# Kernel optimization log

Hardware: AMD Instinct MI355X
Metric: run time of the kernel (lower is better)

The kernel has to match this reference:

```python
import jax, jax.numpy as jnp
import numpy as np

N_NODES = 200000
N_EDGES = 6400000
HIDDEN = 200
N_HID_LAYERS = 6  # 8-layer MLP: in + 6 hidden + out


def setup_inputs() -> dict:
    key = jax.random.key(0)
    ks = jax.random.split(key, 12)
    x = jax.random.normal(ks[0], (N_NODES, 1), dtype=jnp.float32)
    edge_index = jax.random.randint(ks[1], (2, N_EDGES), 0, N_NODES, dtype=jnp.int64)
    # GraphConv(1,1): lin_rel (with bias) applied to aggregated neighbors, lin_root (no bias)
    w_rel = jax.random.normal(ks[2], (1, 1), dtype=jnp.float32)
    b_rel = jax.random.normal(ks[3], (1,), dtype=jnp.float32) * 0.1
    w_root = jax.random.normal(ks[4], (1, 1), dtype=jnp.float32)
    # MLP(1, 200, 1, num_layers=8)
    w_in = jax.random.normal(ks[5], (1, HIDDEN), dtype=jnp.float32) * (1.0 / 1.0)
    b_in = jnp.zeros((HIDDEN,), dtype=jnp.float32)
    w_hid = jax.random.normal(ks[6], (N_HID_LAYERS, HIDDEN, HIDDEN), dtype=jnp.float32) * (1.0 / np.sqrt(HIDDEN))
    b_hid = jnp.zeros((N_HID_LAYERS, HIDDEN), dtype=jnp.float32)
    w_out = jax.random.normal(ks[7], (HIDDEN, 1), dtype=jnp.float32) * (1.0 / np.sqrt(HIDDEN))
    b_out = jnp.zeros((1,), dtype=jnp.float32)
    return {
        "x": x, "edge_index": edge_index,
        "w_rel": w_rel, "b_rel": b_rel, "w_root": w_root,
        "w_in": w_in, "b_in": b_in,
        "w_hid": w_hid, "b_hid": b_hid,
        "w_out": w_out, "b_out": b_out,
    }


def reference(x, edge_index, w_rel, b_rel, w_root, w_in, b_in, w_hid, b_hid, w_out, b_out):
    # GraphConv with sum aggregation: out_i = W_rel @ sum_{j in N(i)} x_j + b_rel + W_root @ x_i
    src = edge_index[0]
    dst = edge_index[1]
    agg = jax.ops.segment_sum(x[src], dst, num_segments=N_NODES)  # [N, 1]
    h = agg @ w_rel + b_rel + x @ w_root                          # [N, 1]
    # 8-layer MLP with ReLU between layers
    h = jax.nn.relu(h @ w_in + b_in)                              # [N, 200]
    for i in range(N_HID_LAYERS):
        h = jax.nn.relu(h @ w_hid[i] + b_hid[i])
    h = h @ w_out + b_out                                         # [N, 1]
    return jax.nn.sigmoid(h)
```

## Files before the change

kernel.cpp:

```cpp
#include <hip/hip_runtime.h>

#define N_NODES 200000
#define N_EDGES 6400000
#define HID 200
#define NREP 8
#define MT 64
#define ASTR 232
#define AELEM (MT * ASTR)
#define WSTR 232
#define WROWS 224
#define WELEMS (WROWS * WSTR)
#define H0ROWS 112
#define H1ROWS 96
#define H0CH (H0ROWS * WSTR * 2 / 16)
#define H1CH (H1ROWS * WSTR * 2 / 16)

#define LDS_WOFF 29696
#define LDS_TOTAL 81664

#define NPART 20
#define PNODES 10000
#define PBLK 50
#define CHUNK_E (N_EDGES / PBLK)
#define APPLY_LDS (PNODES * 4)

typedef float f32x4 __attribute__((ext_vector_type(4)));
typedef _Float16 f16x8 __attribute__((ext_vector_type(8)));
typedef unsigned short u16;
typedef unsigned int u32;

__device__ __align__(16) float g_agg[N_NODES];
__device__ __align__(16) float g_xf8[NREP * N_NODES];
__device__ __align__(16) float g_wf[6 * HID * HID];
__device__ __align__(16) _Float16 g_wph[6 * WELEMS];
__device__ __align__(16) float g_ev[N_EDGES];
__device__ __align__(16) float g_part[NPART * PBLK * PNODES];
__device__ int g_isbf;

__device__ __forceinline__ float bf2f(u16 u) {
  union { u32 i; float f; } v; v.i = ((u32)u) << 16; return v.f;
}
__device__ __forceinline__ u16 f2bf(float f) {
  u32 i = __float_as_uint(f);
  return (u16)((i + 0x7FFFu + ((i >> 16) & 1u)) >> 16);
}
__device__ __forceinline__ float ldf(const void* p, int i, int isbf) {
  return isbf ? bf2f(((const u16*)p)[i]) : ((const float*)p)[i];
}
__device__ __forceinline__ void load_lds16(const void* g, void* l) {
  __builtin_amdgcn_global_load_lds(
      (const __attribute__((address_space(1))) u32*)g,
      (__attribute__((address_space(3))) u32*)l, 16, 0, 0);
}

constexpr int tf1(int m) { return (m & 3) + 1; }
constexpr int tf2(int m) { return ((m >> 2) & 3) + 2; }
constexpr int tg1(int k) { return (k & 7) + 1; }
constexpr int tg2(int k) { return ((k >> 3) & 3) + 1; }
constexpr int tu1(int k) { return ((k * 3) & 7) + 1; }
constexpr int tu2(int k) { return ((k >> 2) & 3) + 2; }
constexpr int tw1(int n) { return ((n * 5) & 7) + 1; }
constexpr int tw2(int n) { return ((n >> 2) & 3) + 1; }
constexpr int calcS(int i, int j) {
  int s = 0;
  for (int k = 0; k < 32; ++k)
    s += (i ? tg2(k) : tg1(k)) * (j ? tu2(k) : tu1(k));
  return s;
}
__device__ __forceinline__ float refD(int m, int n) {
  constexpr int S11 = calcS(0, 0), S12 = calcS(0, 1), S21 = calcS(1, 0), S22 = calcS(1, 1);
  return (float)(tf1(m) * tw1(n) * S11 + tf1(m) * tw2(n) * S12 +
                 tf2(m) * tw1(n) * S21 + tf2(m) * tw2(n) * S22);
}
__device__ int mfma_selftest(int l15, int q) {
  f16x8 av, bv;
#pragma unroll
  for (int j = 0; j < 8; ++j) {
    int k = q * 8 + j;
    av[j] = (_Float16)(float)(tf1(l15) * tg1(k) + tf2(l15) * tg2(k));
    bv[j] = (_Float16)(float)(tu1(k) * tw1(l15) + tu2(k) * tw2(l15));
  }
  f32x4 d = __builtin_amdgcn_mfma_f32_16x16x32_f16(av, bv, (f32x4){0.f, 0.f, 0.f, 0.f}, 0, 0, 0);
  bool ok0 = true, ok1 = true;
#pragma unroll
  for (int r = 0; r < 4; ++r) {
    ok0 = ok0 && (d[r] == refD(q * 4 + r, l15));
    ok1 = ok1 && (d[r] == refD(l15, q * 4 + r));
  }
  return __all(ok0) ? 0 : (__all(ok1) ? 1 : 2);
}

__global__ void sniff_kernel(const u32* __restrict__ xw) {
  int i = threadIdx.x;
  u32 e = (xw[i] >> 7) & 0xFFu;
  unsigned long long b = __ballot(e >= 110u && e <= 135u);
  if (i == 0) g_isbf = (__popcll(b) >= 48) ? 1 : 0;
}

__global__ void prep_kernel(const void* __restrict__ x, const void* __restrict__ w_hid) {
  int t = blockIdx.x * blockDim.x + threadIdx.x;
  int isbf = g_isbf;
  if (t < NREP * N_NODES) {
    int qd = t / N_NODES;
    int node = t - qd * N_NODES;
    g_xf8[t] = ldf(x, node, isbf);
  }
  if (t < 6 * HID * HID) g_wf[t] = ldf(w_hid, t, isbf);
  if (t < 6 * WELEMS) {
    int l = t / WELEMS;
    int r = t - l * WELEMS;
    int n = r / WSTR;
    int k = r - n * WSTR;
    float v = 0.f;
    if (n < HID && k < HID) v = ldf(w_hid, (l * HID + k) * HID + n, isbf);
    g_wph[t] = (_Float16)v;
  }
}

__global__ void gather_kernel(const int* __restrict__ ei) {
  int t = blockIdx.x * blockDim.x + threadIdx.x;
  int e = t * 8;
  int xcc;
  asm volatile("s_getreg_b32 %0, hwreg(HW_REG_XCC_ID)" : "=s"(xcc));
  const float* xf = g_xf8 + (size_t)(xcc & (NREP - 1)) * N_NODES;
  bool is64 = ((ei[1] | ei[3] | ei[5] | ei[7]) == 0);
  int s[8];
  if (is64) {
#pragma unroll
    for (int i = 0; i < 4; ++i) {
      int4 a = *(const int4*)(ei + 2 * e + 4 * i);
      s[2 * i] = a.x; s[2 * i + 1] = a.z;
    }
  } else {
#pragma unroll
    for (int i = 0; i < 2; ++i) {
      int4 a = *(const int4*)(ei + e + 4 * i);
      s[4 * i] = a.x; s[4 * i + 1] = a.y; s[4 * i + 2] = a.z; s[4 * i + 3] = a.w;
    }
  }
  float v[8];
#pragma unroll
  for (int i = 0; i < 8; ++i) v[i] = xf[s[i]];
  *(float4*)(g_ev + e) = (float4){v[0], v[1], v[2], v[3]};
  *(float4*)(g_ev + e + 4) = (float4){v[4], v[5], v[6], v[7]};
}

__global__ __launch_bounds__(256) void apply_kernel(const int* __restrict__ ei) {
  extern __shared__ float part[];
  const int tid = threadIdx.x;
  const int p = blockIdx.x / PBLK;
  const int cb = blockIdx.x - p * PBLK;
  const int lo = p * PNODES;
  float4* pv = (float4*)part;
  for (int c = tid; c < PNODES / 4; c += 256) pv[c] = (float4){0.f, 0.f, 0.f, 0.f};
  __syncthreads();
  const bool is64 = ((ei[1] | ei[3] | ei[5] | ei[7]) == 0);
  const int base = cb * CHUNK_E;
  for (int g = 0; g < CHUNK_E / (256 * 4); ++g) {
    int idx = base + (g * 256 + tid) * 4;
    float4 v = *(const float4*)(g_ev + idx);
    int d0, d1, d2, d3;
    if (is64) {
      int4 b0 = *(const int4*)(ei + 2 * (size_t)N_EDGES + 2 * (size_t)idx);
      int4 b1 = *(const int4*)(ei + 2 * (size_t)N_EDGES + 2 * (size_t)idx + 4);
      d0 = b0.x; d1 = b0.z; d2 = b1.x; d3 = b1.z;
    } else {
      int4 b = *(const int4*)(ei + N_EDGES + idx);
      d0 = b.x; d1 = b.y; d2 = b.z; d3 = b.w;
    }
    unsigned u0 = (unsigned)(d0 - lo), u1 = (unsigned)(d1 - lo);
    unsigned u2 = (unsigned)(d2 - lo), u3 = (unsigned)(d3 - lo);
    if (u0 < PNODES) __hip_atomic_fetch_add(&part[u0], v.x, __ATOMIC_RELAXED, __HIP_MEMORY_SCOPE_WORKGROUP);
    if (u1 < PNODES) __hip_atomic_fetch_add(&part[u1], v.y, __ATOMIC_RELAXED, __HIP_MEMORY_SCOPE_WORKGROUP);
    if (u2 < PNODES) __hip_atomic_fetch_add(&part[u2], v.z, __ATOMIC_RELAXED, __HIP_MEMORY_SCOPE_WORKGROUP);
    if (u3 < PNODES) __hip_atomic_fetch_add(&part[u3], v.w, __ATOMIC_RELAXED, __HIP_MEMORY_SCOPE_WORKGROUP);
  }
  __syncthreads();
  float* gp = g_part + (size_t)blockIdx.x * PNODES;
  for (int c = tid; c < PNODES / 4; c += 256)
    *(float4*)(gp + c * 4) = pv[c];
}

__global__ void reduce_kernel() {
  int n = blockIdx.x * 256 + threadIdx.x;
  if (n >= N_NODES) return;
  int p = n / PNODES;
  int off = n - p * PNODES;
  const float* base = g_part + (size_t)p * PBLK * PNODES + off;
  float s = 0.f;
#pragma unroll
  for (int c = 0; c < PBLK; ++c) s += base[(size_t)c * PNODES];
  g_agg[n] = s;
}

__global__ __launch_bounds__(512, 4) void mlp_kernel(
    const void* __restrict__ w_rel, const void* __restrict__ b_rel, const void* __restrict__ w_root,
    const void* __restrict__ w_in, const void* __restrict__ b_in,
    const void* __restrict__ b_hid, const void* __restrict__ w_out, const void* __restrict__ b_out,
    void* __restrict__ out) {
  extern __shared__ char smem[];
  _Float16* act = (_Float16*)smem;
  _Float16* wlds = (_Float16*)(smem + LDS_WOFF);
  float* h0s = (float*)(smem + LDS_WOFF);

  const int tid = threadIdx.x;
  const int nb = blockIdx.x * MT;
  const int isbf = g_isbf;
  const int lane = tid & 63;
  const int wv = tid >> 6;
  const int l15 = lane & 15;
  const int q = lane >> 4;
  const int band = wv >> 1;
  const int cg = wv & 1;

  const int mode = mfma_selftest(l15, q);

  if (tid < MT) {
    int node = nb + tid;
    h0s[tid] = g_agg[node] * ldf(w_rel, 0, isbf) + ldf(b_rel, 0, isbf) +
               g_xf8[node] * ldf(w_root, 0, isbf);
  }
  __syncthreads();

  if (mode < 2) {
    for (int idx = tid; idx < AELEM; idx += 512) {
      int m = idx / ASTR, j = idx - m * ASTR;
      float v = 0.f;
      if (j < HID) {
        v = h0s[m] * ldf(w_in, j, isbf) + ldf(b_in, j, isbf);
        v = fmaxf(v, 0.f);
      }
      act[idx] = (_Float16)v;
    }

    for (int l = 0; l < 6; ++l) {
      f32x4 acc[7];
#pragma unroll
      for (int n = 0; n < 7; ++n) acc[n] = (f32x4){0.f, 0.f, 0.f, 0.f};

      const _Float16* ap = act + (band * 16 + l15) * ASTR + q * 8;

      __syncthreads();
      {
        const _Float16* wg = g_wph + l * WELEMS;
        for (int c = tid; c < H0CH; c += 512) load_lds16(wg + c * 8, wlds + c * 8);
      }
      __syncthreads();
      if (cg == 0) {
        const _Float16* bp = wlds + l15 * WSTR + q * 8;
#pragma unroll
        for (int ks = 0; ks < 7; ++ks) {
          f16x8 a = *(const f16x8*)(ap + ks * 32);
#pragma unroll
          for (int n = 0; n < 4; ++n) {
            f16x8 b = *(const f16x8*)(bp + n * 16 * WSTR + ks * 32);
            acc[n] = __builtin_amdgcn_mfma_f32_16x16x32_f16(a, b, acc[n], 0, 0, 0);
          }
        }
      } else {
        const _Float16* bp = wlds + (4 * 16 + l15) * WSTR + q * 8;
#pragma unroll
        for (int ks = 0; ks < 7; ++ks) {
          f16x8 a = *(const f16x8*)(ap + ks * 32);
#pragma unroll
          for (int n = 0; n < 3; ++n) {
            f16x8 b = *(const f16x8*)(bp + n * 16 * WSTR + ks * 32);
            acc[n] = __builtin_amdgcn_mfma_f32_16x16x32_f16(a, b, acc[n], 0, 0, 0);
          }
        }
      }

      __syncthreads();
      {
        const _Float16* wg = g_wph + l * WELEMS + H0ROWS * WSTR;
        for (int c = tid; c < H1CH; c += 512) load_lds16(wg + c * 8, wlds + c * 8);
      }
      __syncthreads();
      if (cg == 0) {
        const _Float16* bp = wlds + l15 * WSTR + q * 8;
#pragma unroll
        for (int ks = 0; ks < 7; ++ks) {
          f16x8 a = *(const f16x8*)(ap + ks * 32);
#pragma unroll
          for (int n = 0; n < 3; ++n) {
            f16x8 b = *(const f16x8*)(bp + n * 16 * WSTR + ks * 32);
            acc[4 + n] = __builtin_amdgcn_mfma_f32_16x16x32_f16(a, b, acc[4 + n], 0, 0, 0);
          }
        }
      } else {
        const _Float16* bp = wlds + (3 * 16 + l15) * WSTR + q * 8;
#pragma unroll
        for (int ks = 0; ks < 7; ++ks) {
          f16x8 a = *(const f16x8*)(ap + ks * 32);
#pragma unroll
          for (int n = 0; n < 3; ++n) {
            f16x8 b = *(const f16x8*)(bp + n * 16 * WSTR + ks * 32);
            acc[3 + n] = __builtin_amdgcn_mfma_f32_16x16x32_f16(a, b, acc[3 + n], 0, 0, 0);
          }
        }
      }
      __syncthreads();

      if (cg == 0) {
#pragma unroll
        for (int i = 0; i < 7; ++i) {
          const int gt = (i < 4) ? i : 3 + i;
          const int ctile = gt * 16;
#pragma unroll
          for (int r = 0; r < 4; ++r) {
            int rr = (mode == 0) ? (q * 4 + r) : l15;
            int cc = (mode == 0) ? l15 : (q * 4 + r);
            int row = band * 16 + rr, col = ctile + cc;
            float v = acc[i][r] + ((col < HID) ? ldf(b_hid, l * HID + col, isbf) : 0.f);
            act[row * ASTR + col] = (_Float16)fmaxf(v, 0.f);
          }
        }
      } else {
#pragma unroll
        for (int i = 0; i < 6; ++i) {
          const int gt = (i < 3) ? 4 + i : 7 + i;
          const int ctile = gt * 16;
#pragma unroll
          for (int r = 0; r < 4; ++r) {
            int rr = (mode == 0) ? (q * 4 + r) : l15;
            int cc = (mode == 0) ? l15 : (q * 4 + r);
            int row = band * 16 + rr, col = ctile + cc;
            float v = acc[i][r] + ((col < HID) ? ldf(b_hid, l * HID + col, isbf) : 0.f);
            act[row * ASTR + col] = (_Float16)fmaxf(v, 0.f);
          }
        }
      }
    }

    __syncthreads();
    {
      int m = tid >> 3, c = tid & 7;
      const _Float16* ar = act + m * ASTR;
      float s = 0.f;
#pragma unroll
      for (int j = c * 25; j < c * 25 + 25; ++j)
        s += (float)ar[j] * ldf(w_out, j, isbf);
      s += __shfl_down(s, 4);
      s += __shfl_down(s, 2);
      s += __shfl_down(s, 1);
      if (c == 0) {
        float logit = s + ldf(b_out, 0, isbf);
        float o = 1.f / (1.f + __expf(-logit));
        if (isbf) ((u16*)out)[nb + m] = f2bf(o);
        else ((float*)out)[nb + m] = o;
      }
    }
  } else {
    float(*fA)[201] = (float(*)[201])smem;
    float(*fB)[201] = (float(*)[201])(smem + 32 * 201 * 4);
    float* h0f = (float*)(smem + 64 * 201 * 4);
    for (int p = 0; p < 2; ++p) {
      __syncthreads();
      if (tid < 32) {
        int node = nb + p * 32 + tid;
        h0f[tid] = g_agg[node] * ldf(w_rel, 0, isbf) + ldf(b_rel, 0, isbf) +
                   g_xf8[node] * ldf(w_root, 0, isbf);
      }
      __syncthreads();
      for (int i = tid; i < 32 * HID; i += 512) {
        int mm = i / HID, ff = i - mm * HID;
        float v = h0f[mm] * ldf(w_in, ff, isbf) + ldf(b_in, ff, isbf);
        fA[mm][ff] = v > 0.f ? v : 0.f;
      }
      __syncthreads();
      const int m = tid >> 4, c = tid & 15;
      float(*ain)[201] = fA;
      float(*aout)[201] = fB;
      for (int l = 0; l < 6; ++l) {
        float acc[13];
#pragma unroll
        for (int jj = 0; jj < 13; ++jj) {
          int j = c * 13 + jj;
          acc[jj] = (j < HID) ? ldf(b_hid, l * HID + j, isbf) : 0.f;
        }
        const float* wl = g_wf + l * HID * HID;
        for (int k = 0; k < HID; ++k) {
          float a = ain[m][k];
          const float* wr = wl + k * HID;
#pragma unroll
          for (int jj = 0; jj < 13; ++jj) {
            int j = c * 13 + jj;
            if (j < HID) acc[jj] = fmaf(a, wr[j], acc[jj]);
          }
        }
        __syncthreads();
#pragma unroll
        for (int jj = 0; jj < 13; ++jj) {
          int j = c * 13 + jj;
          if (j < HID) aout[m][j] = fmaxf(acc[jj], 0.f);
        }
        float(*tsw)[201] = ain; ain = aout; aout = tsw;
        __syncthreads();
      }
      float s = 0.f;
      for (int j = c * 13; j < c * 13 + 13 && j < HID; ++j)
        s += ain[m][j] * ldf(w_out, j, isbf);
      s += __shfl_down(s, 8);
      s += __shfl_down(s, 4);
      s += __shfl_down(s, 2);
      s += __shfl_down(s, 1);
      int node = nb + p * 32 + m;
      if (c == 0) {
        float logit = s + ldf(b_out, 0, isbf);
        float o = 1.f / (1.f + __expf(-logit));
        if (isbf) ((u16*)out)[node] = f2bf(o);
        else ((float*)out)[node] = o;
      }
    }
  }
}

extern "C" void kernel_launch(void* const* d_in, const int* in_sizes, int n_in,
                              void* d_out, int out_size, void* d_ws, size_t ws_size,
                              hipStream_t stream) {
  const void* x      = d_in[0];
  const int* ei      = (const int*)d_in[1];
  const void* w_rel  = d_in[2];
  const void* b_rel  = d_in[3];
  const void* w_root = d_in[4];
  const void* w_in   = d_in[5];
  const void* b_in   = d_in[6];
  const void* w_hid  = d_in[7];
  const void* b_hid  = d_in[8];
  const void* w_out  = d_in[9];
  const void* b_out  = d_in[10];
  (void)d_ws; (void)ws_size; (void)in_sizes; (void)n_in; (void)out_size;

  sniff_kernel<<<1, 64, 0, stream>>>((const u32*)x);
  prep_kernel<<<(NREP * N_NODES + 255) / 256, 256, 0, stream>>>(x, w_hid);
  gather_kernel<<<N_EDGES / 8 / 256, 256, 0, stream>>>(ei);
  apply_kernel<<<NPART * PBLK, 256, APPLY_LDS, stream>>>(ei);
  reduce_kernel<<<(N_NODES + 255) / 256, 256, 0, stream>>>();
  mlp_kernel<<<N_NODES / MT, 512, LDS_TOTAL, stream>>>(
      w_rel, b_rel, w_root, w_in, b_in, b_hid, w_out, b_out, d_out);
}
```

Measured before the change: 636.7 us.

## Switch MLP GEMMs to 32x32x16 MFMA with fragment-packed weights and activations

Replaces the 16x16x32 f16 MFMA tiling with 32x32x16 MFMA, splitting the 8 waves into 2 row bands by 4 column groups. Weights are prepacked on the device into a per-lane fragment order so each lane reads a contiguous 16-byte chunk from LDS, and activations are kept in the same packed layout instead of a padded row-major array. The intent is fewer MFMA and LDS instructions per layer with conflict-free LDS reads. In exchange, the epilogue writes scattered 2-byte stores into the packed layout, one of the four column-group waves does only half the MFMA work, and the layout self-test now targets the 32x32 instruction.

Result: faster. 589.9 us (-7.3%).

```diff
diff --git a/kernel.cpp b/kernel.cpp
--- a/kernel.cpp
+++ b/kernel.cpp
@@ -5,18 +5,14 @@
 #define HID 200
 #define NREP 8
 #define MT 64
-#define ASTR 232
-#define AELEM (MT * ASTR)
-#define WSTR 232
-#define WROWS 224
-#define WELEMS (WROWS * WSTR)
-#define H0ROWS 112
-#define H1ROWS 96
-#define H0CH (H0ROWS * WSTR * 2 / 16)
-#define H1CH (H1ROWS * WSTR * 2 / 16)
-
-#define LDS_WOFF 29696
-#define LDS_TOTAL 81664
+
+#define PK_ELEMS (7 * 14 * 512)
+#define PK_HALF  (PK_ELEMS / 2)
+#define STG_CHUNKS (PK_HALF * 2 / 16)
+
+#define LDS_WOFF 28672
+#define LDS_H0S  78848
+#define LDS_TOTAL 79104
 
 #define NPART 20
 #define PNODES 10000
@@ -25,6 +21,7 @@
 #define APPLY_LDS (PNODES * 4)
 
 typedef float f32x4 __attribute__((ext_vector_type(4)));
+typedef float f32x16 __attribute__((ext_vector_type(16)));
 typedef _Float16 f16x8 __attribute__((ext_vector_type(8)));
 typedef unsigned short u16;
 typedef unsigned int u32;
@@ -32,7 +29,7 @@
 __device__ __align__(16) float g_agg[N_NODES];
 __device__ __align__(16) float g_xf8[NREP * N_NODES];
 __device__ __align__(16) float g_wf[6 * HID * HID];
-__device__ __align__(16) _Float16 g_wph[6 * WELEMS];
+__device__ __align__(16) _Float16 g_wpk[6 * PK_ELEMS];
 __device__ __align__(16) float g_ev[N_EDGES];
 __device__ __align__(16) float g_part[NPART * PBLK * PNODES];
 __device__ int g_isbf;
@@ -53,39 +50,44 @@
       (__attribute__((address_space(3))) u32*)l, 16, 0, 0);
 }
 
-constexpr int tf1(int m) { return (m & 3) + 1; }
-constexpr int tf2(int m) { return ((m >> 2) & 3) + 2; }
-constexpr int tg1(int k) { return (k & 7) + 1; }
-constexpr int tg2(int k) { return ((k >> 3) & 3) + 1; }
-constexpr int tu1(int k) { return ((k * 3) & 7) + 1; }
-constexpr int tu2(int k) { return ((k >> 2) & 3) + 2; }
-constexpr int tw1(int n) { return ((n * 5) & 7) + 1; }
-constexpr int tw2(int n) { return ((n >> 2) & 3) + 1; }
-constexpr int calcS(int i, int j) {
+constexpr int sf1(int m) { return (m & 7) + 1; }
+constexpr int sf2(int m) { return ((m >> 3) & 3) + 2; }
+constexpr int sg1(int k) { return (k & 7) + 1; }
+constexpr int sg2(int k) { return ((k >> 3) & 1) + 1; }
+constexpr int su1(int k) { return ((k * 3) & 7) + 1; }
+constexpr int su2(int k) { return ((k >> 2) & 3) + 2; }
+constexpr int sw1(int n) { return ((n * 5) & 7) + 1; }
+constexpr int sw2(int n) { return ((n >> 3) & 3) + 1; }
+constexpr int calcS32(int i, int j) {
   int s = 0;
-  for (int k = 0; k < 32; ++k)
-    s += (i ? tg2(k) : tg1(k)) * (j ? tu2(k) : tu1(k));
+  for (int k = 0; k < 16; ++k)
+    s += (i ? sg2(k) : sg1(k)) * (j ? su2(k) : su1(k));
   return s;
 }
-__device__ __forceinline__ float refD(int m, int n) {
-  constexpr int S11 = calcS(0, 0), S12 = calcS(0, 1), S21 = calcS(1, 0), S22 = calcS(1, 1);
-  return (float)(tf1(m) * tw1(n) * S11 + tf1(m) * tw2(n) * S12 +
-                 tf2(m) * tw1(n) * S21 + tf2(m) * tw2(n) * S22);
-}
-__device__ int mfma_selftest(int l15, int q) {
+__device__ __forceinline__ float refD32(int m, int n) {
+  constexpr int S11 = calcS32(0, 0), S12 = calcS32(0, 1), S21 = calcS32(1, 0), S22 = calcS32(1, 1);
+  return (float)(sf1(m) * sw1(n) * S11 + sf1(m) * sw2(n) * S12 +
+                 sf2(m) * sw1(n) * S21 + sf2(m) * sw2(n) * S22);
+}
+__device__ int mfma_selftest32(int lane) {
+  const int m = lane & 31, kh = lane >> 5;
   f16x8 av, bv;
 #pragma unroll
   for (int j = 0; j < 8; ++j) {
-    int k = q * 8 + j;
-    av[j] = (_Float16)(float)(tf1(l15) * tg1(k) + tf2(l15) * tg2(k));
-    bv[j] = (_Float16)(float)(tu1(k) * tw1(l15) + tu2(k) * tw2(l15));
-  }
-  f32x4 d = __builtin_amdgcn_mfma_f32_16x16x32_f16(av, bv, (f32x4){0.f, 0.f, 0.f, 0.f}, 0, 0, 0);
+    int k = kh * 8 + j;
+    av[j] = (_Float16)(float)(sf1(m) * sg1(k) + sf2(m) * sg2(k));
+    bv[j] = (_Float16)(float)(su1(k) * sw1(m) + su2(k) * sw2(m));
+  }
+  f32x16 z;
+#pragma unroll
+  for (int i = 0; i < 16; ++i) z[i] = 0.f;
+  f32x16 d = __builtin_amdgcn_mfma_f32_32x32x16_f16(av, bv, z, 0, 0, 0);
   bool ok0 = true, ok1 = true;
 #pragma unroll
-  for (int r = 0; r < 4; ++r) {
-    ok0 = ok0 && (d[r] == refD(q * 4 + r, l15));
-    ok1 = ok1 && (d[r] == refD(l15, q * 4 + r));
+  for (int reg = 0; reg < 16; ++reg) {
+    int rr = (reg & 3) + 8 * (reg >> 2) + 4 * kh;
+    ok0 = ok0 && (d[reg] == refD32(rr, m));
+    ok1 = ok1 && (d[reg] == refD32(m, rr));
   }
   return __all(ok0) ? 0 : (__all(ok1) ? 1 : 2);
 }
@@ -106,14 +108,21 @@
     g_xf8[t] = ldf(x, node, isbf);
   }
   if (t < 6 * HID * HID) g_wf[t] = ldf(w_hid, t, isbf);
-  if (t < 6 * WELEMS) {
-    int l = t / WELEMS;
-    int r = t - l * WELEMS;
-    int n = r / WSTR;
-    int k = r - n * WSTR;
-    float v = 0.f;
-    if (n < HID && k < HID) v = ldf(w_hid, (l * HID + k) * HID + n, isbf);
-    g_wph[t] = (_Float16)v;
+  if (t < 6 * PK_ELEMS) {
+    int l = t / PK_ELEMS;
+    int r = t - l * PK_ELEMS;
+    int h = r / PK_HALF;
+    int r2 = r - h * PK_HALF;
+    int tile = r2 / 3584;
+    int r3 = r2 - tile * 3584;
+    int ks7 = r3 >> 9;
+    int r4 = r3 & 511;
+    int ln = r4 >> 3;
+    int j = r4 & 7;
+    int n = tile * 32 + (ln & 31);
+    int k = (h * 7 + ks7) * 16 + (ln >> 5) * 8 + j;
+    float v = (n < HID && k < HID) ? ldf(w_hid, (l * HID + k) * HID + n, isbf) : 0.f;
+    g_wpk[t] = (_Float16)v;
   }
 }
 
@@ -199,21 +208,20 @@
     const void* __restrict__ b_hid, const void* __restrict__ w_out, const void* __restrict__ b_out,
     void* __restrict__ out) {
   extern __shared__ char smem[];
-  _Float16* act = (_Float16*)smem;
-  _Float16* wlds = (_Float16*)(smem + LDS_WOFF);
-  float* h0s = (float*)(smem + LDS_WOFF);
+  _Float16* actp = (_Float16*)smem;
+  _Float16* wbuf = (_Float16*)(smem + LDS_WOFF);
+  float* h0s = (float*)(smem + LDS_H0S);
 
   const int tid = threadIdx.x;
   const int nb = blockIdx.x * MT;
   const int isbf = g_isbf;
   const int lane = tid & 63;
   const int wv = tid >> 6;
-  const int l15 = lane & 15;
-  const int q = lane >> 4;
-  const int band = wv >> 1;
-  const int cg = wv & 1;
-
-  const int mode = mfma_selftest(l15, q);
+  const int band = wv >> 2;
+  const int cg = wv & 3;
+  const int t0 = cg * 2;
+
+  const int mode = mfma_selftest32(lane);
 
   if (tid < MT) {
     int node = nb + tid;
@@ -223,110 +231,98 @@
   __syncthreads();
 
   if (mode < 2) {
-    for (int idx = tid; idx < AELEM; idx += 512) {
-      int m = idx / ASTR, j = idx - m * ASTR;
-      float v = 0.f;
-      if (j < HID) {
-        v = h0s[m] * ldf(w_in, j, isbf) + ldf(b_in, j, isbf);
-        v = fmaxf(v, 0.f);
-      }
-      act[idx] = (_Float16)v;
+    for (int u = tid; u < MT * 28; u += 512) {
+      int m = u / 28, g = u - m * 28;
+      int ks = g >> 1, kh = g & 1;
+      float h0v = h0s[m];
+      f16x8 pv;
+#pragma unroll
+      for (int j = 0; j < 8; ++j) {
+        int col = ks * 16 + kh * 8 + j;
+        float v = 0.f;
+        if (col < HID) v = fmaxf(h0v * ldf(w_in, col, isbf) + ldf(b_in, col, isbf), 0.f);
+        pv[j] = (_Float16)v;
+      }
+      *(f16x8*)(actp + ((m >> 5) * 14 + ks) * 512 + (kh * 32 + (m & 31)) * 8) = pv;
     }
 
     for (int l = 0; l < 6; ++l) {
-      f32x4 acc[7];
-#pragma unroll
-      for (int n = 0; n < 7; ++n) acc[n] = (f32x4){0.f, 0.f, 0.f, 0.f};
-
-      const _Float16* ap = act + (band * 16 + l15) * ASTR + q * 8;
-
+      f32x16 acc0, acc1;
+#pragma unroll
+      for (int i = 0; i < 16; ++i) { acc0[i] = 0.f; acc1[i] = 0.f; }
+
+#pragma unroll
+      for (int h = 0; h < 2; ++h) {
+        __syncthreads();
+        {
+          const _Float16* wg = g_wpk + (size_t)l * PK_ELEMS + h * PK_HALF;
+          for (int c = tid; c < STG_CHUNKS; c += 512) load_lds16(wg + c * 8, wbuf + c * 8);
+        }
+        __syncthreads();
+
+        f16x8 af[7];
+#pragma unroll
+        for (int i = 0; i < 7; ++i)
+          af[i] = *(const f16x8*)(actp + (band * 14 + h * 7 + i) * 512 + lane * 8);
+
+        if (cg < 3) {
+#pragma unroll
+          for (int i = 0; i < 7; ++i) {
+            f16x8 b0 = *(const f16x8*)(wbuf + (t0 * 7 + i) * 512 + lane * 8);
+            f16x8 b1 = *(const f16x8*)(wbuf + ((t0 + 1) * 7 + i) * 512 + lane * 8);
+            acc0 = __builtin_amdgcn_mfma_f32_32x32x16_f16(af[i], b0, acc0, 0, 0, 0);
+            acc1 = __builtin_amdgcn_mfma_f32_32x32x16_f16(af[i], b1, acc1, 0, 0, 0);
+          }
+        } else {
+#pragma unroll
+          for (int i = 0; i < 7; ++i) {
+            f16x8 b0 = *(const f16x8*)(wbuf + (6 * 7 + i) * 512 + lane * 8);
+            acc0 = __builtin_amdgcn_mfma_f32_32x32x16_f16(af[i], b0, acc0, 0, 0, 0);
+          }
+        }
+      }
       __syncthreads();
-      {
-        const _Float16* wg = g_wph + l * WELEMS;
-        for (int c = tid; c < H0CH; c += 512) load_lds16(wg + c * 8, wlds + c * 8);
-      }
-      __syncthreads();
-      if (cg == 0) {
-        const _Float16* bp = wlds + l15 * WSTR + q * 8;
-#pragma unroll
-        for (int ks = 0; ks < 7; ++ks) {
-          f16x8 a = *(const f16x8*)(ap + ks * 32);
-#pragma unroll
-          for (int n = 0; n < 4; ++n) {
-            f16x8 b = *(const f16x8*)(bp + n * 16 * WSTR + ks * 32);
-            acc[n] = __builtin_amdgcn_mfma_f32_16x16x32_f16(a, b, acc[n], 0, 0, 0);
+
+      if (mode == 0) {
+        const int c0 = lane & 31, kh = lane >> 5;
+        {
+          int col = t0 * 32 + c0;
+          float bias = (col < HID) ? ldf(b_hid, l * HID + col, isbf) : 0.f;
+          _Float16* dst = actp + (band * 14 + (col >> 4)) * 512 +
+                          ((col >> 3) & 1) * 256 + (col & 7);
+#pragma unroll
+          for (int reg = 0; reg < 16; ++reg) {
+            int rr = (reg & 3) + 8 * (reg >> 2) + 4 * kh;
+            dst[rr * 8] = (_Float16)fmaxf(acc0[reg] + bias, 0.f);
+          }
+        }
+        if (cg < 3) {
+          int col = (t0 + 1) * 32 + c0;
+          float bias = (col < HID) ? ldf(b_hid, l * HID + col, isbf) : 0.f;
+          _Float16* dst = actp + (band * 14 + (col >> 4)) * 512 +
+                          ((col >> 3) & 1) * 256 + (col & 7);
+#pragma unroll
+          for (int reg = 0; reg < 16; ++reg) {
+            int rr = (reg & 3) + 8 * (reg >> 2) + 4 * kh;
+            dst[rr * 8] = (_Float16)fmaxf(acc1[reg] + bias, 0.f);
           }
         }
       } else {
-        const _Float16* bp = wlds + (4 * 16 + l15) * WSTR + q * 8;
-#pragma unroll
-        for (int ks = 0; ks < 7; ++ks) {
-          f16x8 a = *(const f16x8*)(ap + ks * 32);
-#pragma unroll
-          for (int n = 0; n < 3; ++n) {
-            f16x8 b = *(const f16x8*)(bp + n * 16 * WSTR + ks * 32);
-            acc[n] = __builtin_amdgcn_mfma_f32_16x16x32_f16(a, b, acc[n], 0, 0, 0);
-          }
-        }
-      }
-
-      __syncthreads();
-      {
-        const _Float16* wg = g_wph + l * WELEMS + H0ROWS * WSTR;
-        for (int c = tid; c < H1CH; c += 512) load_lds16(wg + c * 8, wlds + c * 8);
-      }
-      __syncthreads();
-      if (cg == 0) {
-        const _Float16* bp = wlds + l15 * WSTR + q * 8;
-#pragma unroll
-        for (int ks = 0; ks < 7; ++ks) {
-          f16x8 a = *(const f16x8*)(ap + ks * 32);
-#pragma unroll
-          for (int n = 0; n < 3; ++n) {
-            f16x8 b = *(const f16x8*)(bp + n * 16 * WSTR + ks * 32);
-            acc[4 + n] = __builtin_amdgcn_mfma_f32_16x16x32_f16(a, b, acc[4 + n], 0, 0, 0);
-          }
-        }
-      } else {
-        const _Float16* bp = wlds + (3 * 16 + l15) * WSTR + q * 8;
-#pragma unroll
-        for (int ks = 0; ks < 7; ++ks) {
-          f16x8 a = *(const f16x8*)(ap + ks * 32);
-#pragma unroll
-          for (int n = 0; n < 3; ++n) {
-            f16x8 b = *(const f16x8*)(bp + n * 16 * WSTR + ks * 32);
-            acc[3 + n] = __builtin_amdgcn_mfma_f32_16x16x32_f16(a, b, acc[3 + n], 0, 0, 0);
-          }
-        }
-      }
-      __syncthreads();
-
-      if (cg == 0) {
-#pragma unroll
-        for (int i = 0; i < 7; ++i) {
-          const int gt = (i < 4) ? i : 3 + i;
-          const int ctile = gt * 16;
-#pragma unroll
-          for (int r = 0; r < 4; ++r) {
-            int rr = (mode == 0) ? (q * 4 + r) : l15;
-            int cc = (mode == 0) ? l15 : (q * 4 + r);
-            int row = band * 16 + rr, col = ctile + cc;
-            float v = acc[i][r] + ((col < HID) ? ldf(b_hid, l * HID + col, isbf) : 0.f);
-            act[row * ASTR + col] = (_Float16)fmaxf(v, 0.f);
-          }
-        }
-      } else {
-#pragma unroll
-        for (int i = 0; i < 6; ++i) {
-          const int gt = (i < 3) ? 4 + i : 7 + i;
-          const int ctile = gt * 16;
-#pragma unroll
-          for (int r = 0; r < 4; ++r) {
-            int rr = (mode == 0) ? (q * 4 + r) : l15;
-            int cc = (mode == 0) ? l15 : (q * 4 + r);
-            int row = band * 16 + rr, col = ctile + cc;
-            float v = acc[i][r] + ((col < HID) ? ldf(b_hid, l * HID + col, isbf) : 0.f);
-            act[row * ASTR + col] = (_Float16)fmaxf(v, 0.f);
+        const int rr = lane & 31, kh = lane >> 5;
+#pragma unroll
+        for (int reg = 0; reg < 16; ++reg) {
+          int cc = (reg & 3) + 8 * (reg >> 2) + 4 * kh;
+          {
+            int col = t0 * 32 + cc;
+            float v = acc0[reg] + ((col < HID) ? ldf(b_hid, l * HID + col, isbf) : 0.f);
+            actp[(band * 14 + (col >> 4)) * 512 + (((col >> 3) & 1) * 32 + rr) * 8 + (col & 7)] =
+                (_Float16)fmaxf(v, 0.f);
+          }
+          if (cg < 3) {
+            int col = (t0 + 1) * 32 + cc;
+            float v = acc1[reg] + ((col < HID) ? ldf(b_hid, l * HID + col, isbf) : 0.f);
+            actp[(band * 14 + (col >> 4)) * 512 + (((col >> 3) & 1) * 32 + rr) * 8 + (col & 7)] =
+                (_Float16)fmaxf(v, 0.f);
           }
         }
       }
@@ -335,11 +331,13 @@
     __syncthreads();
     {
       int m = tid >> 3, c = tid & 7;
-      const _Float16* ar = act + m * ASTR;
+      const int mb = (m >> 5) * 14, ml = m & 31;
       float s = 0.f;
 #pragma unroll
-      for (int j = c * 25; j < c * 25 + 25; ++j)
-        s += (float)ar[j] * ldf(w_out, j, isbf);
+      for (int j = c * 25; j < c * 25 + 25; ++j) {
+        _Float16 a = actp[(mb + (j >> 4)) * 512 + (((j >> 3) & 1) * 32 + ml) * 8 + (j & 7)];
+        s += (float)a * ldf(w_out, j, isbf);
+      }
       s += __shfl_down(s, 4);
       s += __shfl_down(s, 2);
       s += __shfl_down(s, 1);
```
